# Optimization experiments

Hardware: AMD Instinct MI355X
Metric: run time of the kernel (lower is better)

The kernel has to match this reference:

```python
import jax, jax.numpy as jnp
import numpy as np

CHUNK = 32
FLOOR = 0.01
EPS_MIX = 1e-5
EPS_NORM = 1e-5


def l2norm(x):
    return x / jnp.sqrt(jnp.sum(x * x, -1, keepdims=True) + 1e-12)


def dw_causal_conv(x, w):
    # x: (B, L, C), w: (C, K) depthwise causal conv, tap K-1 is 'current'
    K = w.shape[-1]
    L = x.shape[1]
    xp = jnp.pad(x, ((0, 0), (K - 1, 0), (0, 0)))
    y = jnp.zeros_like(x)
    for t in range(K):
        y = y + xp[:, t:t + L, :] * w[:, t]
    return y


def delta_rule_chunkwise(q, k, v, beta):
    # q,k: (B,H,L,dk), v: (B,H,L,dv), beta: (B,H,L); L % CHUNK == 0
    b, h, L, dk = q.shape
    dv = v.shape[-1]
    c = CHUNK
    n = L // c
    q = l2norm(q)
    k = l2norm(k)
    v = v * beta[..., None]
    kb = k * beta[..., None]
    rs = lambda x: x.reshape(b, h, n, c, -1)
    qc, kc, vc, kbc = rs(q), rs(k), rs(v), rs(kb)
    # in-chunk inverse of (I + tril(K_beta K^T)) via forward substitution
    T = -jnp.einsum('bhnid,bhnjd->bhnij', kbc, kc)
    tri_strict = jnp.tril(jnp.ones((c, c), bool), -1)
    T = jnp.where(tri_strict, T, 0.0)
    for i in range(1, c):
        T = T.at[..., i, :i].add(
            jnp.einsum('bhnj,bhnji->bhni', T[..., i, :], T[..., :, :i]))
    T = T + jnp.eye(c, dtype=T.dtype)
    u = jnp.einsum('bhnij,bhnjd->bhnid', T, vc)
    w = jnp.einsum('bhnij,bhnjd->bhnid', T, kbc)
    mask_incl = jnp.tril(jnp.ones((c, c), bool), 0)

    def step(S, inp):
        qi, ki, ui, wi = inp  # each (b,h,c,d)
        attn = jnp.einsum('bhid,bhjd->bhij', qi, ki)
        attn = jnp.where(mask_incl, attn, 0.0)
        u_i = ui - jnp.einsum('bhik,bhkd->bhid', wi, S)
        o_i = jnp.einsum('bhik,bhkd->bhid', qi, S) + jnp.einsum('bhij,bhjd->bhid', attn, u_i)
        S = S + jnp.einsum('bhci,bhcd->bhid', ki, u_i)
        return S, o_i

    S0 = jnp.zeros((b, h, dk, dv), q.dtype)
    xs = tuple(jnp.moveaxis(a, 2, 0) for a in (qc, kc, u, w))
    S, o = jax.lax.scan(step, S0, xs)
    o = jnp.moveaxis(o, 0, 2).reshape(b, h, L, dv)
    return o, S


def setup_inputs() -> dict:
    key = jax.random.key(0)
    B, L, D, H = 4, 4096, 1024, 4
    dh = D // H  # 256
    ks = jax.random.split(key, 20)
    s = 1.0 / np.sqrt(D)
    inp = {
        'hidden_states': jax.random.normal(ks[0], (B, L, D), jnp.float32),
        'Wq': jax.random.normal(ks[1], (D, D), jnp.float32) * s,
        'Wk': jax.random.normal(ks[2], (D, D), jnp.float32) * s,
        'Wv': jax.random.normal(ks[3], (D, D), jnp.float32) * s,
        'Wb': jax.random.normal(ks[4], (D, H), jnp.float32) * s,
        'conv_q_w': jax.random.normal(ks[5], (D, 4), jnp.float32) * 0.5,
        'conv_k_w': jax.random.normal(ks[6], (D, 4), jnp.float32) * 0.5,
        'conv_v_w': jax.random.normal(ks[7], (D, 4), jnp.float32) * 0.5,
        'local_w': (jax.random.normal(ks[8], (H * dh, 7), jnp.float32) / np.sqrt(7.0)).at[:, -1].add(1.0),
        'mid_w': (jax.random.normal(ks[9], (H * dh, 25), jnp.float32) / np.sqrt(25.0)).at[:, -1].add(1.0),
        'r_w1': jax.random.normal(ks[10], (D + 14 * H, 2 * (D + 14 * H)), jnp.float32) / np.sqrt(D + 14 * H),
        'r_b1': jnp.zeros((2 * (D + 14 * H),), jnp.float32),
        'r_w2': jax.random.normal(ks[11], (2 * (D + 14 * H), H * 4), jnp.float32) / np.sqrt(2.0 * (D + 14 * H)),
        'r_b2': jnp.zeros((H, 4), jnp.float32).at[:, 2:].set(0.7).reshape(-1),
        'mix_w': jnp.ones((H, dh), jnp.float32),
        'onorm_w': jnp.ones((dh,), jnp.float32),
        'Wo': jax.random.normal(ks[12], (D, D), jnp.float32) * s,
    }
    return inp


def reference(hidden_states, Wq, Wk, Wv, Wb, conv_q_w, conv_k_w, conv_v_w,
              local_w, mid_w, r_w1, r_b1, r_w2, r_b2, mix_w, onorm_w, Wo):
    B, L, D = hidden_states.shape
    H = mix_w.shape[0]
    dh = mix_w.shape[1]
    # projections + short causal depthwise convs with SiLU (qk_activation='silu')
    q = jax.nn.silu(dw_causal_conv(hidden_states @ Wq, conv_q_w))
    k = jax.nn.silu(dw_causal_conv(hidden_states @ Wk, conv_k_w))
    v = jax.nn.silu(dw_causal_conv(hidden_states @ Wv, conv_v_w))
    q4 = q.reshape(B, L, H, dh)
    k4 = k.reshape(B, L, H, dh)
    v4 = v.reshape(B, L, H, dh)
    beta = jax.nn.sigmoid(hidden_states @ Wb)  # (B,L,H)
    delta_out, _ = delta_rule_chunkwise(
        jnp.transpose(q4, (0, 2, 1, 3)), jnp.transpose(k4, (0, 2, 1, 3)),
        jnp.transpose(v4, (0, 2, 1, 3)), jnp.transpose(beta, (0, 2, 1)))
    delta_out = jnp.transpose(delta_out, (0, 2, 1, 3))  # (B,L,H,dh)
    v_direct = v4
    vflat = v4.reshape(B, L, H * dh)
    local_out = dw_causal_conv(vflat, local_w).reshape(B, L, H, dh)
    mid_out = dw_causal_conv(vflat, mid_w).reshape(B, L, H, dh)
    outs = [local_out, mid_out, delta_out, v_direct]
    # router stats: per-head mean/var of each path + pairwise mean dots
    feats = []
    for o_ in outs:
        feats.append(o_.mean(-1))
        feats.append(jnp.var(o_, -1, ddof=1))
    for i in range(4):
        for j in range(i + 1, 4):
            feats.append((outs[i] * outs[j]).mean(-1))
    router_feat = jnp.concatenate([hidden_states] + feats, axis=-1)  # (B,L,D+14H)
    h1 = jax.nn.silu(router_feat @ r_w1 + r_b1)
    logits = (h1 @ r_w2 + r_b2).reshape(B, L, H, 4)
    p = jax.nn.softmax(logits, -1)
    p = p * (1.0 - 4.0 * FLOOR) + FLOOR  # probability floor
    mixed = sum(p[..., i:i + 1] * outs[i] for i in range(4))  # (B,L,H,dh)
    # MixNorm: per-token per-head RMSNorm with (H,dh) affine
    rms = jnp.sqrt(jnp.mean(mixed * mixed, -1, keepdims=True) + EPS_MIX)
    mixed = mixed / rms * mix_w
    # output RMSNorm (per head_v_dim)
    rms2 = jnp.sqrt(jnp.mean(mixed * mixed, -1, keepdims=True) + EPS_NORM)
    o_n = mixed / rms2 * onorm_w
    return o_n.reshape(B, L, H * dh) @ Wo
```

## Files before the change

kernel.cpp:

```cpp
#include <hip/hip_runtime.h>
#include <cstdint>
#include <cstddef>

typedef unsigned short u16;
typedef __bf16 bf16x8 __attribute__((ext_vector_type(8)));
typedef float    f32x4 __attribute__((ext_vector_type(4)));
typedef unsigned short u16x8 __attribute__((ext_vector_type(8)));
typedef unsigned short u16x4 __attribute__((ext_vector_type(4)));

#define MFMA16(a,b,c) __builtin_amdgcn_mfma_f32_16x16x32_bf16(a,b,c,0,0,0)

__device__ __forceinline__ float bf2f(u16 u){ return __uint_as_float(((unsigned)u)<<16); }
__device__ __forceinline__ u16 f2bf(float f){
  unsigned x = __float_as_uint(f);
  unsigned r = x + 0x7fffu + ((x>>16)&1u);
  return (u16)(r>>16);
}
__device__ __forceinline__ float wred(float v){
  #pragma unroll
  for (int o=32;o;o>>=1) v += __shfl_xor(v,o,64);
  return v;
}
__device__ __forceinline__ float siluf(float x){ return x/(1.f+__expf(-x)); }

__global__ __launch_bounds__(256) void k_zero(float* __restrict__ p, int n){
  int i = blockIdx.x*256 + threadIdx.x;
  if (i < n) p[i] = 0.f;
}

__global__ __launch_bounds__(256) void k_cvt(const float* __restrict__ src,
                                             u16* __restrict__ dst, int n){
  int i = (blockIdx.x*256 + threadIdx.x)*4;
  if (i < n){
    float4 f = *(const float4*)(src + i);
    u16x4 o; o[0]=f2bf(f.x); o[1]=f2bf(f.y); o[2]=f2bf(f.z); o[3]=f2bf(f.w);
    *(u16x4*)(dst + i) = o;
  }
}

__global__ __launch_bounds__(256) void k_tr(const float* __restrict__ src, u16* __restrict__ dst,
                                            int R, int C, int Rp, int Cp){
  __shared__ float t[32][33];
  int n0 = blockIdx.x*32, k0 = blockIdx.y*32;
  int tx = threadIdx.x & 31, ty = threadIdx.x >> 5;
  #pragma unroll
  for (int j=0;j<4;j++){
    int k = k0 + ty + j*8, nn = n0 + tx;
    t[ty + j*8][tx] = (k < R && nn < C) ? src[k*C + nn] : 0.f;
  }
  __syncthreads();
  #pragma unroll
  for (int j=0;j<4;j++){
    int nn = n0 + ty + j*8, k = k0 + tx;
    dst[nn*Rp + k] = f2bf(t[tx][ty + j*8]);
  }
}

__global__ __launch_bounds__(256) void k_pad_w2t(const float* __restrict__ src, u16* __restrict__ dst){
  int k = blockIdx.x*256 + threadIdx.x;
  int j = blockIdx.y;
  if (k < 2176) dst[j*2176 + k] = (k < 2160) ? f2bf(src[k*16 + j]) : (u16)0;
}
__global__ __launch_bounds__(256) void k_pad_b1(const float* __restrict__ src, float* __restrict__ dst){
  int i = blockIdx.x*256 + threadIdx.x;
  if (i < 2176) dst[i] = (i<2160) ? src[i] : 0.f;
}

__global__ __launch_bounds__(256) void k_trk(const u16* __restrict__ kn, u16* __restrict__ kTb){
  __shared__ u16 vs[32][264];
  const int g = blockIdx.x;
  const int bh = g >> 7, nc = g & 127;
  const int b = bh >> 2, h = bh & 3;
  const int tid = threadIdx.x;
  const int rr = tid >> 3, cb = (tid & 7) * 32;
  const u16* src = kn + (size_t)(b*4096 + nc*32 + rr)*1024 + h*256 + cb;
  #pragma unroll
  for (int v=0; v<4; ++v){
    u16x8 x = *(const u16x8*)(src + v*8);
    *(u16x8*)&vs[rr][cb + v*8] = x;
  }
  __syncthreads();
  u16* dst = kTb + ((size_t)g*256 + tid)*32;
  #pragma unroll
  for (int v=0; v<4; ++v){
    u16x8 o;
    #pragma unroll
    for (int e=0; e<8; e++) o[e] = vs[v*8 + e][tid];
    *(u16x8*)(dst + v*8) = o;
  }
}

__global__ __launch_bounds__(256,2) void k_gemm(
    const u16* __restrict__ A, const u16* __restrict__ Bt, void* __restrict__ Cvp,
    int M, int N, int K, int out_f32)
{
  __shared__ u16 As[2][128*64];
  __shared__ u16 Bs[2][128*64];
  const int tid = threadIdx.x;
  const int lane = tid & 63, wv = tid >> 6;
  const int wm = (wv>>1)*64, wn = (wv&1)*64;
  const int r15 = lane & 15, q4 = lane >> 4;
  const int bm0 = blockIdx.y*128, bn0 = blockIdx.x*128;
  const int srow = tid>>3, sch = tid&7;
  const int nk = K >> 6;

  const f32x4 fz = {0.f,0.f,0.f,0.f};
  f32x4 acc[4][4];
  #pragma unroll
  for (int i=0;i<4;i++){
    #pragma unroll
    for (int j=0;j<4;j++) acc[i][j] = fz;
  }

  {
    u16x8 ca[4], cb[4];
    #pragma unroll
    for (int i=0;i<4;i++){
      int r = i*32 + srow;
      ca[i] = *(const u16x8*)(A  + (size_t)(bm0+r)*K + sch*8);
      cb[i] = *(const u16x8*)(Bt + (size_t)(bn0+r)*K + sch*8);
    }
    #pragma unroll
    for (int i=0;i<4;i++){
      int r = i*32 + srow;
      int byt = r*128 + ((sch ^ (r&7))*16);
      *(u16x8*)((char*)(&As[0][0]) + byt) = ca[i];
      *(u16x8*)((char*)(&Bs[0][0]) + byt) = cb[i];
    }
  }
  int cur = 0;
  for (int t=0; t<nk; ++t){
    u16x8 na[4], nb[4];
    if (t+1 < nk){
      const int kt = (t+1)<<6;
      #pragma unroll
      for (int i=0;i<4;i++){
        int r = i*32 + srow;
        na[i] = *(const u16x8*)(A  + (size_t)(bm0+r)*K + kt + sch*8);
        nb[i] = *(const u16x8*)(Bt + (size_t)(bn0+r)*K + kt + sch*8);
      }
    }
    __syncthreads();
    const u16* as_ = &As[cur][0];
    const u16* bs_ = &Bs[cur][0];
    #pragma unroll
    for (int kk=0; kk<2; ++kk){
      bf16x8 av[4], bv[4];
      #pragma unroll
      for (int mi=0;mi<4;mi++){
        int row = wm + mi*16 + r15;
        int ch  = kk*4 + q4;
        av[mi] = *(const bf16x8*)((const char*)as_ + row*128 + ((ch ^ (row&7))*16));
      }
      #pragma unroll
      for (int ni=0;ni<4;ni++){
        int row = wn + ni*16 + r15;
        int ch  = kk*4 + q4;
        bv[ni] = *(const bf16x8*)((const char*)bs_ + row*128 + ((ch ^ (row&7))*16));
      }
      #pragma unroll
      for (int mi=0;mi<4;mi++){
        #pragma unroll
        for (int ni=0;ni<4;ni++)
          acc[mi][ni] = MFMA16(av[mi], bv[ni], acc[mi][ni]);
      }
    }
    if (t+1 < nk){
      #pragma unroll
      for (int i=0;i<4;i++){
        int r = i*32 + srow;
        int byt = r*128 + ((sch ^ (r&7))*16);
        *(u16x8*)((char*)(&As[cur^1][0]) + byt) = na[i];
        *(u16x8*)((char*)(&Bs[cur^1][0]) + byt) = nb[i];
      }
    }
    cur ^= 1;
  }
  float* Cf = (float*)Cvp;
  u16*  Cb2 = (u16*)Cvp;
  #pragma unroll
  for (int mi=0;mi<4;mi++){
    #pragma unroll
    for (int ni=0;ni<4;ni++){
      int gr = bm0 + wm + mi*16 + q4*4;
      int gc = bn0 + wn + ni*16 + r15;
      #pragma unroll
      for (int rg=0; rg<4; ++rg){
        float v = acc[mi][ni][rg];
        size_t off = (size_t)(gr+rg)*N + gc;
        if (out_f32) Cf[off] = v; else Cb2[off] = f2bf(v);
      }
    }
  }
}

union SMu {
  struct { u16 As[2][128*64]; u16 Bs[2][128*64]; } g;
  u16 h1s[128][136];
};
__global__ __launch_bounds__(256,2) void k_gemm_router(
    const u16* __restrict__ A, const u16* __restrict__ Bt,
    const float* __restrict__ bias, const u16* __restrict__ w2t,
    float* __restrict__ logits)
{
  __shared__ SMu sm;
  const int tid = threadIdx.x;
  const int lane = tid & 63, wv = tid >> 6;
  const int wm = (wv>>1)*64, wn = (wv&1)*64;
  const int r15 = lane & 15, q4 = lane >> 4;
  const int bm0 = blockIdx.y*128, bn0 = blockIdx.x*128;
  const int srow = tid>>3, sch = tid&7;
  const int K = 1088, nk = 17;

  const f32x4 fz = {0.f,0.f,0.f,0.f};
  f32x4 acc[4][4];
  #pragma unroll
  for (int i=0;i<4;i++){
    #pragma unroll
    for (int j=0;j<4;j++) acc[i][j] = fz;
  }
  {
    u16x8 ca[4], cb[4];
    #pragma unroll
    for (int i=0;i<4;i++){
      int r = i*32 + srow;
      ca[i] = *(const u16x8*)(A  + (size_t)(bm0+r)*K + sch*8);
      cb[i] = *(const u16x8*)(Bt + (size_t)(bn0+r)*K + sch*8);
    }
    #pragma unroll
    for (int i=0;i<4;i++){
      int r = i*32 + srow;
      int byt = r*128 + ((sch ^ (r&7))*16);
      *(u16x8*)((char*)(&sm.g.As[0][0]) + byt) = ca[i];
      *(u16x8*)((char*)(&sm.g.Bs[0][0]) + byt) = cb[i];
    }
  }
  int cur = 0;
  for (int t=0; t<nk; ++t){
    u16x8 na[4], nb[4];
    if (t+1 < nk){
      const int kt = (t+1)<<6;
      #pragma unroll
      for (int i=0;i<4;i++){
        int r = i*32 + srow;
        na[i] = *(const u16x8*)(A  + (size_t)(bm0+r)*K + kt + sch*8);
        nb[i] = *(const u16x8*)(Bt + (size_t)(bn0+r)*K + kt + sch*8);
      }
    }
    __syncthreads();
    const u16* as_ = &sm.g.As[cur][0];
    const u16* bs_ = &sm.g.Bs[cur][0];
    #pragma unroll
    for (int kk=0; kk<2; ++kk){
      bf16x8 av[4], bv[4];
      #pragma unroll
      for (int mi=0;mi<4;mi++){
        int row = wm + mi*16 + r15;
        int ch  = kk*4 + q4;
        av[mi] = *(const bf16x8*)((const char*)as_ + row*128 + ((ch ^ (row&7))*16));
      }
      #pragma unroll
      for (int ni=0;ni<4;ni++){
        int row = wn + ni*16 + r15;
        int ch  = kk*4 + q4;
        bv[ni] = *(const bf16x8*)((const char*)bs_ + row*128 + ((ch ^ (row&7))*16));
      }
      #pragma unroll
      for (int mi=0;mi<4;mi++){
        #pragma unroll
        for (int ni=0;ni<4;ni++)
          acc[mi][ni] = MFMA16(av[mi], bv[ni], acc[mi][ni]);
      }
    }
    if (t+1 < nk){
      #pragma unroll
      for (int i=0;i<4;i++){
        int r = i*32 + srow;
        int byt = r*128 + ((sch ^ (r&7))*16);
        *(u16x8*)((char*)(&sm.g.As[cur^1][0]) + byt) = na[i];
        *(u16x8*)((char*)(&sm.g.Bs[cur^1][0]) + byt) = nb[i];
      }
    }
    cur ^= 1;
  }
  __syncthreads();
  #pragma unroll
  for (int mi=0;mi<4;mi++){
    #pragma unroll
    for (int ni=0;ni<4;ni++){
      int lr = wm + mi*16 + q4*4;
      int lc = wn + ni*16 + r15;
      float bv_ = bias[bn0 + lc];
      #pragma unroll
      for (int rg=0; rg<4; ++rg)
        sm.h1s[lr+rg][lc] = f2bf(siluf(acc[mi][ni][rg] + bv_));
    }
  }
  __syncthreads();
  f32x4 lacc[2] = {fz, fz};
  #pragma unroll
  for (int rt=0; rt<2; ++rt){
    #pragma unroll
    for (int ks=0; ks<4; ++ks){
      bf16x8 a = *(const bf16x8*)((const char*)&sm.h1s[wv*32 + rt*16 + r15][0] + ks*64 + q4*16);
      bf16x8 b = *(const bf16x8*)(w2t + r15*2176 + bn0 + ks*32 + q4*8);
      lacc[rt] = MFMA16(a, b, lacc[rt]);
    }
  }
  #pragma unroll
  for (int rt=0; rt<2; ++rt){
    #pragma unroll
    for (int rg=0; rg<4; ++rg){
      int m = bm0 + wv*32 + rt*16 + q4*4 + rg;
      atomicAdd(&logits[m*16 + r15], lacc[rt][rg]);
    }
  }
}

__global__ __launch_bounds__(256) void k_softm(float* __restrict__ p, const float* __restrict__ b2){
  int m = blockIdx.x*256 + threadIdx.x;
  float l[16];
  #pragma unroll
  for (int j=0;j<16;j++) l[j] = p[m*16+j] + b2[j];
  #pragma unroll
  for (int hh=0;hh<4;hh++){
    float l0=l[hh*4+0], l1=l[hh*4+1], l2=l[hh*4+2], l3=l[hh*4+3];
    float mx = fmaxf(fmaxf(l0,l1),fmaxf(l2,l3));
    float e0=__expf(l0-mx), e1=__expf(l1-mx), e2=__expf(l2-mx), e3=__expf(l3-mx);
    float iv = 1.f/(e0+e1+e2+e3);
    p[m*16+hh*4+0]=e0*iv*0.96f+0.01f;
    p[m*16+hh*4+1]=e1*iv*0.96f+0.01f;
    p[m*16+hh*4+2]=e2*iv*0.96f+0.01f;
    p[m*16+hh*4+3]=e3*iv*0.96f+0.01f;
  }
}

__global__ __launch_bounds__(256) void k_beta(const u16* __restrict__ Xb,
                                              const float* __restrict__ Wb,
                                              float* __restrict__ beta){
  int m = blockIdx.x*4 + (threadIdx.x>>6);
  int lane = threadIdx.x & 63;
  float a0=0.f,a1=0.f,a2=0.f,a3=0.f;
  #pragma unroll 4
  for (int i=0;i<16;i++){
    int k = lane + i*64;
    float x = bf2f(Xb[m*1024 + k]);
    float4 wr = *(const float4*)(Wb + k*4);
    a0 += x*wr.x; a1 += x*wr.y; a2 += x*wr.z; a3 += x*wr.w;
  }
  a0 = wred(a0); a1 = wred(a1); a2 = wred(a2); a3 = wred(a3);
  if (lane == 0){
    beta[m*4+0] = 1.f/(1.f+__expf(-a0));
    beta[m*4+1] = 1.f/(1.f+__expf(-a1));
    beta[m*4+2] = 1.f/(1.f+__expf(-a2));
    beta[m*4+3] = 1.f/(1.f+__expf(-a3));
  }
}

__global__ __launch_bounds__(256) void k_conv(const u16* __restrict__ raw,
                                              const float* __restrict__ cw,
                                              u16* __restrict__ outp, int do_norm){
  const int m = blockIdx.x;
  const int tid = threadIdx.x, lane = tid&63, hh = tid>>6;
  const int l = m & 4095;
  const int cbase = hh*256 + lane*4;
  float x[4][4];
  #pragma unroll
  for (int j=0;j<4;j++){
    if (l >= j){
      u16x4 xv = *(const u16x4*)(raw + (m-j)*1024 + cbase);
      #pragma unroll
      for (int e=0;e<4;e++) x[j][e] = bf2f(xv[e]);
    } else {
      #pragma unroll
      for (int e=0;e<4;e++) x[j][e] = 0.f;
    }
  }
  float y[4]; float ss = 0.f;
  #pragma unroll
  for (int e=0;e<4;e++){
    int c = cbase + e;
    float yy = x[0][e]*cw[c*4+3] + x[1][e]*cw[c*4+2] + x[2][e]*cw[c*4+1] + x[3][e]*cw[c*4+0];
    yy = siluf(yy);
    y[e] = yy; ss += yy*yy;
  }
  if (do_norm){
    ss = wred(ss);
    float sc = rsqrtf(ss + 1e-12f);
    #pragma unroll
    for (int e=0;e<4;e++) y[e] *= sc;
  }
  u16x4 o;
  #pragma unroll
  for (int e=0;e<4;e++) o[e] = f2bf(y[e]);
  *(u16x4*)(outp + m*1024 + cbase) = o;
}

__global__ __launch_bounds__(256) void k_localmid(const u16* __restrict__ v,
                                                  const float* __restrict__ lw,
                                                  const float* __restrict__ mw,
                                                  u16* __restrict__ lo, u16* __restrict__ mo){
  __shared__ u16 vs[56][256];
  const int lt0 = blockIdx.x*32;
  const int b = blockIdx.y;
  const int c0 = blockIdx.z*256;
  const int tid = threadIdx.x;
  #pragma unroll
  for (int i=0;i<7;i++){
    int flat = tid + i*256;
    int row = flat >> 5;
    int cc = (flat & 31)*8;
    int tok = lt0 - 24 + row;
    u16x8 val = {0,0,0,0,0,0,0,0};
    if (tok >= 0) val = *(const u16x8*)(v + (b*4096 + tok)*1024 + c0 + cc);
    *(u16x8*)&vs[row][cc] = val;
  }
  __syncthreads();
  const int c = tid;
  float lwr[7], mwr[25];
  #pragma unroll
  for (int i=0;i<7;i++) lwr[i] = lw[(c0+c)*7 + i];
  #pragma unroll
  for (int i=0;i<25;i++) mwr[i] = mw[(c0+c)*25 + i];
  for (int lt=0; lt<32; ++lt){
    float a7=0.f, a25=0.f;
    #pragma unroll
    for (int t=0;t<25;t++) a25 += bf2f(vs[lt+t][c]) * mwr[t];
    #pragma unroll
    for (int t=0;t<7;t++)  a7  += bf2f(vs[18+lt+t][c]) * lwr[t];
    int m = b*4096 + lt0 + lt;
    lo[m*1024 + c0 + c] = f2bf(a7);
    mo[m*1024 + c0 + c] = f2bf(a25);
  }
}

__global__ __launch_bounds__(256,2) void k_chunk(
    const u16* __restrict__ qn, const u16* __restrict__ kn, const u16* __restrict__ v,
    const float* __restrict__ beta, u16* __restrict__ u_, u16* __restrict__ w_,
    u16* __restrict__ attnb)
{
  const int chk = blockIdx.x;
  const int nc = chk & 127;
  const int bh = chk >> 7;
  const int b = bh >> 2, h = bh & 3;
  const int tok0 = b*4096 + nc*32;
  const int tid = threadIdx.x, lane = tid&63, wv = tid>>6;
  const int r15 = lane&15, q4 = lane>>4;

  __shared__ u16 kbT[256][40];
  __shared__ u16 vbT[256][40];
  __shared__ float Tm[4][32][33];
  __shared__ u16 Xs[32][40];

  {
    int rr = tid >> 3;
    int cb = (tid & 7)*32;
    float bt = beta[(tok0 + rr)*4 + h];
    const u16* ksrc = kn + (tok0+rr)*1024 + h*256 + cb;
    const u16* vsrc = v  + (tok0+rr)*1024 + h*256 + cb;
    #pragma unroll
    for (int vvv=0; vvv<4; ++vvv){
      u16x8 kx = *(const u16x8*)(ksrc + vvv*8);
      u16x8 vx = *(const u16x8*)(vsrc + vvv*8);
      #pragma unroll
      for (int e=0;e<8;e++){
        kbT[cb + vvv*8 + e][rr] = f2bf(bf2f(kx[e]) * bt);
        vbT[cb + vvv*8 + e][rr] = f2bf(bf2f(vx[e]) * bt);
      }
    }
  }
  {
    const int i0 = (wv>>1)*16, j0 = (wv&1)*16;
    float bi = beta[(tok0 + i0 + r15)*4 + h];
    f32x4 tacc = {0.f,0.f,0.f,0.f};
    #pragma unroll
    for (int ks=0; ks<8; ++ks){
      u16x8 ar = *(const u16x8*)(kn + (tok0 + i0 + r15)*1024 + h*256 + ks*32 + q4*8);
      union { u16x8 u; bf16x8 bf; } au;
      #pragma unroll
      for (int e=0;e<8;e++) au.u[e] = f2bf(bf2f(ar[e]) * bi);
      bf16x8 bv = *(const bf16x8*)(kn + (tok0 + j0 + r15)*1024 + h*256 + ks*32 + q4*8);
      tacc = MFMA16(au.bf, bv, tacc);
    }
    #pragma unroll
    for (int rg=0; rg<4; ++rg){
      int i = i0 + q4*4 + rg, j = j0 + r15;
      float val = (i > j) ? -tacc[rg] : 0.f;
      Tm[0][i][j] = val;
      Tm[2][i][j] = val + ((i==j)?1.f:0.f);
    }
  }
  __syncthreads();
  int cbuf = 0, cx = 2;
  const int ii = tid >> 3, jj = (tid&7)*4;
  for (int s=0; s<4; ++s){
    int nb = cbuf^1, nx = cx^1;
    {
      float o0=0.f,o1=0.f,o2=0.f,o3=0.f;
      for (int k=0;k<32;k++){
        float a = Tm[cbuf][ii][k];
        o0 += a*Tm[cbuf][k][jj+0]; o1 += a*Tm[cbuf][k][jj+1];
        o2 += a*Tm[cbuf][k][jj+2]; o3 += a*Tm[cbuf][k][jj+3];
      }
      Tm[nb][ii][jj+0]=o0; Tm[nb][ii][jj+1]=o1; Tm[nb][ii][jj+2]=o2; Tm[nb][ii][jj+3]=o3;
    }
    __syncthreads();
    {
      float o0=Tm[cx][ii][jj+0], o1=Tm[cx][ii][jj+1], o2=Tm[cx][ii][jj+2], o3=Tm[cx][ii][jj+3];
      for (int k=0;k<32;k++){
        float a = Tm[nb][ii][k];
        o0 += a*Tm[cx][k][jj+0]; o1 += a*Tm[cx][k][jj+1];
        o2 += a*Tm[cx][k][jj+2]; o3 += a*Tm[cx][k][jj+3];
      }
      Tm[nx][ii][jj+0]=o0; Tm[nx][ii][jj+1]=o1; Tm[nx][ii][jj+2]=o2; Tm[nx][ii][jj+3]=o3;
    }
    __syncthreads();
    cbuf = nb; cx = nx;
  }
  {
    #pragma unroll
    for (int e=0;e<4;e++) Xs[ii][jj+e] = f2bf(Tm[cx][ii][jj+e]);
  }
  __syncthreads();
  {
    #pragma unroll
    for (int nt=0; nt<4; ++nt){
      int n0 = wv*64 + nt*16;
      #pragma unroll
      for (int mt=0; mt<2; ++mt){
        bf16x8 a = *(const bf16x8*)((const char*)&Xs[mt*16 + r15][0] + q4*16);
        bf16x8 bu = *(const bf16x8*)((const char*)&vbT[n0 + r15][0] + q4*16);
        bf16x8 bw = *(const bf16x8*)((const char*)&kbT[n0 + r15][0] + q4*16);
        f32x4 ua = {0.f,0.f,0.f,0.f};
        f32x4 wa = {0.f,0.f,0.f,0.f};
        ua = MFMA16(a, bu, ua);
        wa = MFMA16(a, bw, wa);
        #pragma unroll
        for (int rg=0;rg<4;rg++){
          int row = mt*16 + q4*4 + rg;
          int col = n0 + r15;
          u_[(chk*32 + row)*256 + col] = f2bf(ua[rg]);
          w_[(chk*32 + row)*256 + col] = f2bf(wa[rg]);
        }
      }
    }
  }
  {
    const int i0 = (wv>>1)*16, j0 = (wv&1)*16;
    f32x4 aacc = {0.f,0.f,0.f,0.f};
    #pragma unroll
    for (int ks=0;ks<8;++ks){
      bf16x8 a = *(const bf16x8*)(qn + (tok0 + i0 + r15)*1024 + h*256 + ks*32 + q4*8);
      bf16x8 bv = *(const bf16x8*)(kn + (tok0 + j0 + r15)*1024 + h*256 + ks*32 + q4*8);
      aacc = MFMA16(a, bv, aacc);
    }
    #pragma unroll
    for (int rg=0;rg<4;rg++){
      int i = i0 + q4*4 + rg, j = j0 + r15;
      attnb[chk*1024 + i*32 + j] = f2bf((i>=j)? aacc[rg] : 0.f);
    }
  }
}

struct ScanCtx { u16x8 kf[4]; u16x8 wf[8]; u16x8 at; u16 uv[4]; };

#define SBAR() do{ asm volatile("s_waitcnt lgkmcnt(0)" ::: "memory"); \
                   __builtin_amdgcn_s_barrier(); \
                   asm volatile("" ::: "memory"); }while(0)

#define SPREF(C, CHK) { \
  const u16* kp = kTb + ((size_t)(CHK)*256 + wv*64 + r15)*32 + q4*8; \
  _Pragma("unroll") for (int mt=0;mt<4;++mt) C.kf[mt] = *(const u16x8*)(kp + mt*512); \
  const u16* wp = w_ + ((size_t)(CHK)*32 + tm*16 + r15)*256 + q4*8; \
  _Pragma("unroll") for (int ks=0;ks<8;++ks) C.wf[ks] = *(const u16x8*)(wp + ks*32); \
  C.at = *(const u16x8*)(attnb + (size_t)(CHK)*1024 + (tm*16 + r15)*32 + q4*8); \
  const u16* up = u_ + ((size_t)(CHK)*32 + tm*16 + q4*4)*256 + dv0 + tn*16 + r15; \
  _Pragma("unroll") for (int rg=0;rg<4;++rg) C.uv[rg] = up[rg*256]; \
}

#define SBODY(C, N, NC, CB, NB) { \
  const int chkn_ = chkbase + (((NC)+1 < 128) ? (NC)+1 : 127); \
  SPREF(N, chkn_); \
  u16x8 qf[8]; \
  { const u16* qp = qn + (size_t)(tokbase + (NC)*32 + tm*16 + r15)*1024 + h*256 + q4*8; \
    _Pragma("unroll") for (int ks=0;ks<8;++ks) qf[ks] = *(const u16x8*)(qp + ks*32); } \
  bf16x8 sf[8]; \
  _Pragma("unroll") for (int ks=0;ks<8;++ks) \
    sf[ks] = *(const bf16x8*)((const char*)&Sb[CB][tn*16 + r15][0] + ks*64 + q4*16); \
  f32x4 ua = fz, ub = fz; \
  _Pragma("unroll") for (int ks=0;ks<8;ks+=2){ \
    ua = MFMA16(*(const bf16x8*)&C.wf[ks],   sf[ks],   ua); \
    ub = MFMA16(*(const bf16x8*)&C.wf[ks+1], sf[ks+1], ub); } \
  { u16x4 pk; \
    _Pragma("unroll") for (int rg=0;rg<4;++rg) pk[rg] = f2bf(bf2f(C.uv[rg]) - ua[rg] - ub[rg]); \
    *(u16x4*)&uT[tn*16 + r15][tm*16 + q4*4] = pk; } \
  SBAR(); \
  bf16x8 bu0 = *(const bf16x8*)((const char*)&uT[r15][0] + q4*16); \
  bf16x8 bu1 = *(const bf16x8*)((const char*)&uT[16 + r15][0] + q4*16); \
  f32x4 oa = fz, ob = fz; \
  _Pragma("unroll") for (int ks=0;ks<8;ks+=2){ \
    oa = MFMA16(*(const bf16x8*)&qf[ks],   sf[ks],   oa); \
    ob = MFMA16(*(const bf16x8*)&qf[ks+1], sf[ks+1], ob); } \
  oa = MFMA16(*(const bf16x8*)&C.at, (tn ? bu1 : bu0), oa); \
  _Pragma("unroll") for (int rg=0;rg<4;++rg) \
    od[(size_t)(tokbase + (NC)*32 + tm*16 + q4*4 + rg)*1024 + h*256 + dv0 + tn*16 + r15] = f2bf(oa[rg] + ob[rg]); \
  _Pragma("unroll") for (int mt=0;mt<4;++mt){ \
    Sacc[mt][0] = MFMA16(*(const bf16x8*)&C.kf[mt], bu0, Sacc[mt][0]); \
    Sacc[mt][1] = MFMA16(*(const bf16x8*)&C.kf[mt], bu1, Sacc[mt][1]); } \
  _Pragma("unroll") for (int mt=0;mt<4;++mt){ \
    _Pragma("unroll") for (int ntl=0;ntl<2;++ntl){ \
      u16x4 pk; \
      _Pragma("unroll") for (int rg=0;rg<4;++rg) pk[rg] = f2bf(Sacc[mt][ntl][rg]); \
      *(u16x4*)&Sb[NB][ntl*16 + r15][wv*64 + mt*16 + q4*4] = pk; } } \
  SBAR(); \
}

__global__ __launch_bounds__(256,1) void k_scan(
    const u16* __restrict__ qn, const u16* __restrict__ kTb,
    const u16* __restrict__ u_, const u16* __restrict__ w_,
    const u16* __restrict__ attnb, u16* __restrict__ od)
{
  const int bid = blockIdx.x;
  const int bh  = (bid & 7) | (((bid >> 3) & 1) << 3);
  const int dv0 = (bid >> 4) * 32;
  const int b = bh >> 2, h = bh & 3;
  const int tid = threadIdx.x, lane = tid & 63, wv = tid >> 6;
  const int tm = wv >> 1, tn = wv & 1;
  const int r15 = lane & 15, q4 = lane >> 4;
  const int chkbase = bh * 128;
  const int tokbase = b * 4096;

  __shared__ u16 Sb[2][32][264];
  __shared__ u16 uT[32][40];

  for (int i = tid; i < 2*32*264; i += 256) (&Sb[0][0][0])[i] = 0;
  const f32x4 fz = {0.f,0.f,0.f,0.f};
  f32x4 Sacc[4][2];
  #pragma unroll
  for (int a_=0;a_<4;a_++){
    #pragma unroll
    for (int b_=0;b_<2;b_++) Sacc[a_][b_] = fz;
  }
  ScanCtx cA, cB;
  SPREF(cA, chkbase);
  __syncthreads();

  for (int nc = 0; nc < 128; nc += 2){
    SBODY(cA, cB, nc,   0, 1)
    SBODY(cB, cA, nc+1, 1, 0)
  }
}

__global__ __launch_bounds__(256) void k_feats(
    const float* __restrict__ Xf, const u16* __restrict__ lo, const u16* __restrict__ mo,
    const u16* __restrict__ de, const u16* __restrict__ vv, u16* __restrict__ feat)
{
  const int m = blockIdx.x;
  const int tid = threadIdx.x, lane = tid & 63, hh = tid >> 6;
  {
    float4 xv = *(const float4*)(Xf + m*1024 + tid*4);
    u16x4 o; o[0]=f2bf(xv.x); o[1]=f2bf(xv.y); o[2]=f2bf(xv.z); o[3]=f2bf(xv.w);
    *(u16x4*)(feat + m*1088 + tid*4) = o;
  }
  if (tid < 8) feat[m*1088 + 1080 + tid] = 0;
  const int base = m*1024 + hh*256 + lane*4;
  u16x4 a0 = *(const u16x4*)(lo + base);
  u16x4 a1 = *(const u16x4*)(mo + base);
  u16x4 a2 = *(const u16x4*)(de + base);
  u16x4 a3 = *(const u16x4*)(vv + base);
  float s[14];
  #pragma unroll
  for (int i=0;i<14;i++) s[i]=0.f;
  #pragma unroll
  for (int e=0;e<4;e++){
    float L = bf2f(a0[e]), Mm = bf2f(a1[e]), D = bf2f(a2[e]), V = bf2f(a3[e]);
    s[0]+=L; s[1]+=L*L; s[2]+=Mm; s[3]+=Mm*Mm; s[4]+=D; s[5]+=D*D; s[6]+=V; s[7]+=V*V;
    s[8]+=L*Mm; s[9]+=L*D; s[10]+=L*V; s[11]+=Mm*D; s[12]+=Mm*V; s[13]+=D*V;
  }
  #pragma unroll
  for (int i=0;i<14;i++) s[i] = wred(s[i]);
  if (lane == 0){
    const float inv = 1.f/256.f, invv = 1.f/255.f;
    u16* fb = feat + m*1088 + 1024;
    float mn[4] = {s[0]*inv, s[2]*inv, s[4]*inv, s[6]*inv};
    float vr[4] = {(s[1]-256.f*mn[0]*mn[0])*invv, (s[3]-256.f*mn[1]*mn[1])*invv,
                   (s[5]-256.f*mn[2]*mn[2])*invv, (s[7]-256.f*mn[3]*mn[3])*invv};
    #pragma unroll
    for (int i=0;i<4;i++){ fb[(2*i)*4 + hh] = f2bf(mn[i]); fb[(2*i+1)*4 + hh] = f2bf(vr[i]); }
    #pragma unroll
    for (int i=0;i<6;i++) fb[(8+i)*4 + hh] = f2bf(s[8+i]*inv);
  }
}

__global__ __launch_bounds__(256) void k_mix(
    const u16* __restrict__ lo, const u16* __restrict__ mo, const u16* __restrict__ de,
    const u16* __restrict__ vv, const float* __restrict__ p,
    const float* __restrict__ mixw, const float* __restrict__ onw, u16* __restrict__ on)
{
  const int m = blockIdx.x;
  const int tid = threadIdx.x, lane = tid&63, hh = tid>>6;
  const int dbase = lane*4;
  const int base = m*1024 + hh*256 + dbase;
  float4 pv = *(const float4*)(p + m*16 + hh*4);
  u16x4 a0 = *(const u16x4*)(lo + base);
  u16x4 a1 = *(const u16x4*)(mo + base);
  u16x4 a2 = *(const u16x4*)(de + base);
  u16x4 a3 = *(const u16x4*)(vv + base);
  float g[4]; float ss = 0.f;
  #pragma unroll
  for (int e=0;e<4;e++){
    float x = pv.x*bf2f(a0[e]) + pv.y*bf2f(a1[e]) + pv.z*bf2f(a2[e]) + pv.w*bf2f(a3[e]);
    g[e]=x; ss += x*x;
  }
  ss = wred(ss);
  float r1 = rsqrtf(ss*(1.f/256.f) + 1e-5f);
  float ss2 = 0.f;
  #pragma unroll
  for (int e=0;e<4;e++){ g[e] = g[e]*r1*mixw[hh*256 + dbase + e]; ss2 += g[e]*g[e]; }
  ss2 = wred(ss2);
  float r2 = rsqrtf(ss2*(1.f/256.f) + 1e-5f);
  u16x4 o;
  #pragma unroll
  for (int e=0;e<4;e++) o[e] = f2bf(g[e]*r2*onw[dbase + e]);
  *(u16x4*)(on + base) = o;
}

extern "C" void kernel_launch(void* const* d_in, const int* in_sizes, int n_in,
                              void* d_out, int out_size, void* d_ws, size_t ws_size,
                              hipStream_t stream)
{
  const float* X   = (const float*)d_in[0];
  const float* Wq  = (const float*)d_in[1];
  const float* Wk  = (const float*)d_in[2];
  const float* Wv  = (const float*)d_in[3];
  const float* Wb  = (const float*)d_in[4];
  const float* cqw = (const float*)d_in[5];
  const float* ckw = (const float*)d_in[6];
  const float* cvw = (const float*)d_in[7];
  const float* lw  = (const float*)d_in[8];
  const float* mw  = (const float*)d_in[9];
  const float* rw1 = (const float*)d_in[10];
  const float* rb1 = (const float*)d_in[11];
  const float* rw2 = (const float*)d_in[12];
  const float* rb2 = (const float*)d_in[13];
  const float* mixw= (const float*)d_in[14];
  const float* onw = (const float*)d_in[15];
  const float* Wo  = (const float*)d_in[16];

  char* ws = (char*)d_ws;
  const size_t SLOT = 33554432;
  char* s0 = ws;
  char* s1 = ws + 1*SLOT;
  char* s2 = ws + 2*SLOT;
  char* s3 = ws + 3*SLOT;
  char* s4 = ws + 4*SLOT;
  char* s5 = ws + 5*SLOT;
  char* s6 = ws + 6*SLOT;
  char* ext = ws + 7*SLOT;
  u16*   attb  = (u16*)(ext);
  float* pb    = (float*)(ext + 4194304);
  float* betab = (float*)(ext + 4194304 + 1048576);
  char*  wsp   = ext + 4194304 + 1048576 + 262144;
  u16* Wqt = (u16*)(wsp);
  u16* Wkt = (u16*)(wsp + 2097152);
  u16* Wvt = (u16*)(wsp + 2*2097152);
  u16* Wot = (u16*)(wsp + 3*2097152);
  u16* w1t = (u16*)(wsp + 4*2097152);
  u16* w2t = (u16*)(wsp + 4*2097152 + 4734976);
  float* b1p = (float*)(wsp + 4*2097152 + 4734976 + 69632);

  u16* Xb    = (u16*)s0;
  u16* rawb  = (u16*)s1;
  u16* qnb   = (u16*)s2;
  u16* knb   = (u16*)s3;
  u16* vpb   = (u16*)s4;
  u16* ub    = (u16*)s0;
  u16* wbuf  = (u16*)s1;
  u16* odb   = (u16*)s5;
  u16* kTbp  = (u16*)s6;
  u16* lob   = (u16*)s2;
  u16* mob   = (u16*)s3;
  u16* featb = (u16*)s0;
  u16* onb   = (u16*)s0;

  k_zero<<<1024,256,0,stream>>>(pb, 262144);
  k_cvt<<<16384,256,0,stream>>>(X, Xb, 16777216);
  k_tr<<<dim3(32,32),256,0,stream>>>(Wq, Wqt, 1024,1024,1024,1024);
  k_tr<<<dim3(32,32),256,0,stream>>>(Wk, Wkt, 1024,1024,1024,1024);
  k_tr<<<dim3(32,32),256,0,stream>>>(Wv, Wvt, 1024,1024,1024,1024);
  k_tr<<<dim3(32,32),256,0,stream>>>(Wo, Wot, 1024,1024,1024,1024);
  k_tr<<<dim3(68,34),256,0,stream>>>(rw1, w1t, 1080,2160,1088,2176);
  k_pad_w2t<<<dim3(9,16),256,0,stream>>>(rw2, w2t);
  k_pad_b1<<<9,256,0,stream>>>(rb1, b1p);
  k_gemm<<<dim3(8,128),256,0,stream>>>(Xb, Wqt, rawb, 16384,1024,1024, 0);
  k_conv<<<16384,256,0,stream>>>(rawb, cqw, qnb, 1);
  k_gemm<<<dim3(8,128),256,0,stream>>>(Xb, Wkt, rawb, 16384,1024,1024, 0);
  k_conv<<<16384,256,0,stream>>>(rawb, ckw, knb, 1);
  k_gemm<<<dim3(8,128),256,0,stream>>>(Xb, Wvt, rawb, 16384,1024,1024, 0);
  k_conv<<<16384,256,0,stream>>>(rawb, cvw, vpb, 0);
  k_beta<<<4096,256,0,stream>>>(Xb, Wb, betab);
  k_chunk<<<2048,256,0,stream>>>(qnb, knb, vpb, betab, ub, wbuf, attb);
  k_trk<<<2048,256,0,stream>>>(knb, kTbp);
  k_scan<<<128,256,0,stream>>>(qnb, kTbp, ub, wbuf, attb, odb);
  k_localmid<<<dim3(128,4,4),256,0,stream>>>(vpb, lw, mw, lob, mob);
  k_feats<<<16384,256,0,stream>>>(X, lob, mob, odb, vpb, featb);
  k_gemm_router<<<dim3(17,128),256,0,stream>>>(featb, w1t, b1p, w2t, pb);
  k_softm<<<64,256,0,stream>>>(pb, rb2);
  k_mix<<<16384,256,0,stream>>>(lob, mob, odb, vpb, pb, mixw, onw, onb);
  k_gemm<<<dim3(8,128),256,0,stream>>>(onb, Wot, d_out, 16384,1024,1024, 1);
}
```

Before: 1.149 ms.

## Merge 32-token chunks into 128-token superchunks for delta-rule scan

Adds compose kernels that merge adjacent chunk-local u/w (WY) representations hierarchically, 32 to 64 to 128, so the sequential scan runs 32 steps of 128 tokens instead of 128 steps of 32. A new kernel computes the causal 128x128 q·k attention as lower-triangular 16x16 tiles, and the scan is split into 256 blocks of 16 value columns for more parallelism. The serial dependency chain of the recurrent state shrinks, in exchange for extra compose passes, more bf16 rounding in the composed u/w, and a reworked workspace layout that reuses the ext region for the transposed Wq/Wk/Wv weights.

```diff
diff --git a/kernel.cpp b/kernel.cpp
--- a/kernel.cpp
+++ b/kernel.cpp
@@ -111,7 +111,6 @@
     #pragma unroll
     for (int j=0;j<4;j++) acc[i][j] = fz;
   }
-
   {
     u16x8 ca[4], cb[4];
     #pragma unroll
@@ -436,8 +435,7 @@
 
 __global__ __launch_bounds__(256,2) void k_chunk(
     const u16* __restrict__ qn, const u16* __restrict__ kn, const u16* __restrict__ v,
-    const float* __restrict__ beta, u16* __restrict__ u_, u16* __restrict__ w_,
-    u16* __restrict__ attnb)
+    const float* __restrict__ beta, u16* __restrict__ u_, u16* __restrict__ w_)
 {
   const int chk = blockIdx.x;
   const int nc = chk & 127;
@@ -545,109 +543,195 @@
       }
     }
   }
+}
+
+__global__ __launch_bounds__(256,2) void k_attn128(const u16* __restrict__ qn,
+                                                   const u16* __restrict__ kn,
+                                                   u16* __restrict__ att){
+  const int g = blockIdx.x;
+  const int bh = g >> 5, sc = g & 31;
+  const int b = bh >> 2, h = bh & 3;
+  const int tid = threadIdx.x, lane = tid&63, wv = tid>>6;
+  const int r15 = lane&15, q4 = lane>>4;
+  const int tok0 = b*4096 + sc*128;
+  const f32x4 fz = {0.f,0.f,0.f,0.f};
+  u16* base = att + (size_t)g*36*256;
+  #pragma unroll
+  for (int ti=0; ti<8; ++ti){
+    #pragma unroll
+    for (int tj=0; tj<=ti; ++tj){
+      if (((ti+tj)&3) != wv) continue;
+      f32x4 acc = fz;
+      const u16* qp = qn + (size_t)(tok0 + ti*16 + r15)*1024 + h*256 + q4*8;
+      const u16* kp = kn + (size_t)(tok0 + tj*16 + r15)*1024 + h*256 + q4*8;
+      #pragma unroll
+      for (int ks=0; ks<8; ++ks)
+        acc = MFMA16(*(const bf16x8*)(qp + ks*32), *(const bf16x8*)(kp + ks*32), acc);
+      u16* op = base + (size_t)(((ti*(ti+1))>>1) + tj)*256;
+      #pragma unroll
+      for (int rg=0; rg<4; ++rg){
+        float vv = acc[rg];
+        if (ti==tj && r15 > q4*4+rg) vv = 0.f;
+        op[(q4*4+rg)*16 + r15] = f2bf(vv);
+      }
+    }
+  }
+}
+
+template<int HS>
+__global__ __launch_bounds__(256,1) void k_compose(const u16* __restrict__ kn,
+                                                   u16* __restrict__ u_,
+                                                   u16* __restrict__ w_){
+  const int g = blockIdx.x;
+  const int ppb = 2048/HS;
+  const int bh = g / ppb, pr = g % ppb;
+  const int b = bh>>2, h = bh&3;
+  const int ta = pr*2*HS, tb2 = ta + HS;
+  const int tid = threadIdx.x, lane = tid&63, wv = tid>>6;
+  const int r15 = lane&15, q4 = lane>>4;
+  __shared__ u16 uaT[256][HS+8];
+  __shared__ u16 waT[256][HS+8];
+  __shared__ u16 Ms[HS][HS+8];
+  const f32x4 fz = {0.f,0.f,0.f,0.f};
   {
-    const int i0 = (wv>>1)*16, j0 = (wv&1)*16;
-    f32x4 aacc = {0.f,0.f,0.f,0.f};
-    #pragma unroll
-    for (int ks=0;ks<8;++ks){
-      bf16x8 a = *(const bf16x8*)(qn + (tok0 + i0 + r15)*1024 + h*256 + ks*32 + q4*8);
-      bf16x8 bv = *(const bf16x8*)(kn + (tok0 + j0 + r15)*1024 + h*256 + ks*32 + q4*8);
-      aacc = MFMA16(a, bv, aacc);
-    }
-    #pragma unroll
-    for (int rg=0;rg<4;rg++){
-      int i = i0 + q4*4 + rg, j = j0 + r15;
-      attnb[chk*1024 + i*32 + j] = f2bf((i>=j)? aacc[rg] : 0.f);
-    }
-  }
-}
-
-struct ScanCtx { u16x8 kf[4]; u16x8 wf[8]; u16x8 at; u16 uv[4]; };
+    const int tpr = 256/HS;
+    const int jr = tid / tpr;
+    const int dg = (tid % tpr) * HS;
+    const u16* us = u_ + (size_t)(bh*4096 + ta + jr)*256 + dg;
+    const u16* wsc = w_ + (size_t)(bh*4096 + ta + jr)*256 + dg;
+    #pragma unroll
+    for (int e0=0; e0<HS; e0+=8){
+      u16x8 xu = *(const u16x8*)(us + e0);
+      u16x8 xw = *(const u16x8*)(wsc + e0);
+      #pragma unroll
+      for (int e=0;e<8;e++){ uaT[dg+e0+e][jr] = xu[e]; waT[dg+e0+e][jr] = xw[e]; }
+    }
+  }
+  constexpr int NT = HS/16;
+  for (int t = wv; t < NT*NT; t += 4){
+    int ti = t / NT, tj = t % NT;
+    f32x4 acc = fz;
+    const u16* ap = w_ + (size_t)(bh*4096 + tb2 + ti*16 + r15)*256 + q4*8;
+    const u16* bp = kn + (size_t)(b*4096 + ta + tj*16 + r15)*1024 + h*256 + q4*8;
+    #pragma unroll
+    for (int ks=0; ks<8; ++ks)
+      acc = MFMA16(*(const bf16x8*)(ap + ks*32), *(const bf16x8*)(bp + ks*32), acc);
+    #pragma unroll
+    for (int rg=0; rg<4; ++rg)
+      Ms[ti*16 + q4*4 + rg][tj*16 + r15] = f2bf(acc[rg]);
+  }
+  __syncthreads();
+  for (int t = wv; t < NT*16; t += 4){
+    int ti = t >> 4, nj = t & 15;
+    f32x4 aU = fz, aW = fz;
+    #pragma unroll
+    for (int js=0; js<HS/32; ++js){
+      bf16x8 a  = *(const bf16x8*)((const char*)&Ms[ti*16 + r15][0] + js*64 + q4*16);
+      bf16x8 bu = *(const bf16x8*)((const char*)&uaT[nj*16 + r15][0] + js*64 + q4*16);
+      bf16x8 bw = *(const bf16x8*)((const char*)&waT[nj*16 + r15][0] + js*64 + q4*16);
+      aU = MFMA16(a, bu, aU);
+      aW = MFMA16(a, bw, aW);
+    }
+    #pragma unroll
+    for (int rg=0; rg<4; ++rg){
+      size_t off = (size_t)(bh*4096 + tb2 + ti*16 + q4*4 + rg)*256 + nj*16 + r15;
+      u_[off] = f2bf(bf2f(u_[off]) - aU[rg]);
+      w_[off] = f2bf(bf2f(w_[off]) - aW[rg]);
+    }
+  }
+}
+
+struct Pref { u16x8 wf[2][8]; u16x4 uv[2]; };
 
 #define SBAR() do{ asm volatile("s_waitcnt lgkmcnt(0)" ::: "memory"); \
                    __builtin_amdgcn_s_barrier(); \
                    asm volatile("" ::: "memory"); }while(0)
 
-#define SPREF(C, CHK) { \
-  const u16* kp = kTb + ((size_t)(CHK)*256 + wv*64 + r15)*32 + q4*8; \
-  _Pragma("unroll") for (int mt=0;mt<4;++mt) C.kf[mt] = *(const u16x8*)(kp + mt*512); \
-  const u16* wp = w_ + ((size_t)(CHK)*32 + tm*16 + r15)*256 + q4*8; \
-  _Pragma("unroll") for (int ks=0;ks<8;++ks) C.wf[ks] = *(const u16x8*)(wp + ks*32); \
-  C.at = *(const u16x8*)(attnb + (size_t)(CHK)*1024 + (tm*16 + r15)*32 + q4*8); \
-  const u16* up = u_ + ((size_t)(CHK)*32 + tm*16 + q4*4)*256 + dv0 + tn*16 + r15; \
-  _Pragma("unroll") for (int rg=0;rg<4;++rg) C.uv[rg] = up[rg*256]; \
-}
-
-#define SBODY(C, N, NC, CB, NB) { \
-  const int chkn_ = chkbase + (((NC)+1 < 128) ? (NC)+1 : 127); \
-  SPREF(N, chkn_); \
-  u16x8 qf[8]; \
-  { const u16* qp = qn + (size_t)(tokbase + (NC)*32 + tm*16 + r15)*1024 + h*256 + q4*8; \
-    _Pragma("unroll") for (int ks=0;ks<8;++ks) qf[ks] = *(const u16x8*)(qp + ks*32); } \
+#define SPREF128(C, SC) { \
+  _Pragma("unroll") for (int rt=0; rt<2; ++rt){ \
+    const u16* wp = w_ + (size_t)(ubase + (SC)*128 + (wv*2+rt)*16 + r15)*256 + q4*8; \
+    _Pragma("unroll") for (int ks=0; ks<8; ++ks) C.wf[rt][ks] = *(const u16x8*)(wp + ks*32); \
+    const u16* up = u_ + (size_t)(ubase + (SC)*128 + (wv*2+rt)*16 + q4*4)*256 + dv0 + r15; \
+    u16x4 t_; \
+    _Pragma("unroll") for (int rg=0; rg<4; ++rg) t_[rg] = up[rg*256]; \
+    C.uv[rt] = t_; } }
+
+#define SBODY128(C, N, SC, CB, NB) { \
+  { const int scn = ((SC)+1 < 32) ? (SC)+1 : 31; SPREF128(N, scn); } \
+  u16x8 kf[4][4]; \
+  _Pragma("unroll") for (int mt=0; mt<4; ++mt) \
+    _Pragma("unroll") for (int sl=0; sl<4; ++sl) \
+      kf[mt][sl] = *(const u16x8*)(kTb + ((size_t)(chkbase + (SC)*4 + sl)*256 + wv*64 + mt*16 + r15)*32 + q4*8); \
+  u16x8 at[2][4]; u16x8 qf[2][8]; \
+  _Pragma("unroll") for (int rt=0; rt<2; ++rt){ \
+    const int R = wv*2+rt; \
+    const u16* ab = att + (size_t)((bh*32 + (SC))*36 + ((R*(R+1))>>1))*256 + r15*16 + (q4&1)*8; \
+    _Pragma("unroll") for (int js=0; js<4; ++js){ \
+      if (js <= (R>>1)){ \
+        int tj = 2*js + (q4>>1); \
+        u16x8 z = {0,0,0,0,0,0,0,0}; \
+        at[rt][js] = (tj <= R) ? *(const u16x8*)(ab + (size_t)tj*256) : z; } } \
+    const u16* qp = qn + (size_t)(qbase + (SC)*128 + R*16 + r15)*1024 + h*256 + q4*8; \
+    _Pragma("unroll") for (int ks=0; ks<8; ++ks) qf[rt][ks] = *(const u16x8*)(qp + ks*32); } \
   bf16x8 sf[8]; \
-  _Pragma("unroll") for (int ks=0;ks<8;++ks) \
-    sf[ks] = *(const bf16x8*)((const char*)&Sb[CB][tn*16 + r15][0] + ks*64 + q4*16); \
-  f32x4 ua = fz, ub = fz; \
-  _Pragma("unroll") for (int ks=0;ks<8;ks+=2){ \
-    ua = MFMA16(*(const bf16x8*)&C.wf[ks],   sf[ks],   ua); \
-    ub = MFMA16(*(const bf16x8*)&C.wf[ks+1], sf[ks+1], ub); } \
-  { u16x4 pk; \
-    _Pragma("unroll") for (int rg=0;rg<4;++rg) pk[rg] = f2bf(bf2f(C.uv[rg]) - ua[rg] - ub[rg]); \
-    *(u16x4*)&uT[tn*16 + r15][tm*16 + q4*4] = pk; } \
+  _Pragma("unroll") for (int ks=0; ks<8; ++ks) \
+    sf[ks] = *(const bf16x8*)((const char*)&Sb[CB][r15][0] + ks*64 + q4*16); \
+  _Pragma("unroll") for (int rt=0; rt<2; ++rt){ \
+    f32x4 ua = fz; \
+    _Pragma("unroll") for (int ks=0; ks<8; ++ks) ua = MFMA16(*(const bf16x8*)&C.wf[rt][ks], sf[ks], ua); \
+    u16x4 pk; \
+    _Pragma("unroll") for (int rg=0; rg<4; ++rg) pk[rg] = f2bf(bf2f(C.uv[rt][rg]) - ua[rg]); \
+    *(u16x4*)&uT[r15][(wv*2+rt)*16 + q4*4] = pk; } \
   SBAR(); \
-  bf16x8 bu0 = *(const bf16x8*)((const char*)&uT[r15][0] + q4*16); \
-  bf16x8 bu1 = *(const bf16x8*)((const char*)&uT[16 + r15][0] + q4*16); \
-  f32x4 oa = fz, ob = fz; \
-  _Pragma("unroll") for (int ks=0;ks<8;ks+=2){ \
-    oa = MFMA16(*(const bf16x8*)&qf[ks],   sf[ks],   oa); \
-    ob = MFMA16(*(const bf16x8*)&qf[ks+1], sf[ks+1], ob); } \
-  oa = MFMA16(*(const bf16x8*)&C.at, (tn ? bu1 : bu0), oa); \
-  _Pragma("unroll") for (int rg=0;rg<4;++rg) \
-    od[(size_t)(tokbase + (NC)*32 + tm*16 + q4*4 + rg)*1024 + h*256 + dv0 + tn*16 + r15] = f2bf(oa[rg] + ob[rg]); \
-  _Pragma("unroll") for (int mt=0;mt<4;++mt){ \
-    Sacc[mt][0] = MFMA16(*(const bf16x8*)&C.kf[mt], bu0, Sacc[mt][0]); \
-    Sacc[mt][1] = MFMA16(*(const bf16x8*)&C.kf[mt], bu1, Sacc[mt][1]); } \
-  _Pragma("unroll") for (int mt=0;mt<4;++mt){ \
-    _Pragma("unroll") for (int ntl=0;ntl<2;++ntl){ \
-      u16x4 pk; \
-      _Pragma("unroll") for (int rg=0;rg<4;++rg) pk[rg] = f2bf(Sacc[mt][ntl][rg]); \
-      *(u16x4*)&Sb[NB][ntl*16 + r15][wv*64 + mt*16 + q4*4] = pk; } } \
-  SBAR(); \
-}
-
-__global__ __launch_bounds__(256,1) void k_scan(
+  bf16x8 bu[4]; \
+  _Pragma("unroll") for (int sl=0; sl<4; ++sl) \
+    bu[sl] = *(const bf16x8*)((const char*)&uT[r15][0] + sl*64 + q4*16); \
+  _Pragma("unroll") for (int rt=0; rt<2; ++rt){ \
+    const int R = wv*2+rt; \
+    f32x4 oa = fz; \
+    _Pragma("unroll") for (int ks=0; ks<8; ++ks) oa = MFMA16(*(const bf16x8*)&qf[rt][ks], sf[ks], oa); \
+    _Pragma("unroll") for (int js=0; js<4; ++js) \
+      if (js <= (R>>1)) oa = MFMA16(*(const bf16x8*)&at[rt][js], bu[js], oa); \
+    _Pragma("unroll") for (int rg=0; rg<4; ++rg) \
+      od[(size_t)(qbase + (SC)*128 + R*16 + q4*4 + rg)*1024 + h*256 + dv0 + r15] = f2bf(oa[rg]); } \
+  _Pragma("unroll") for (int mt=0; mt<4; ++mt){ \
+    _Pragma("unroll") for (int sl=0; sl<4; ++sl) \
+      Sacc[mt] = MFMA16(*(const bf16x8*)&kf[mt][sl], bu[sl], Sacc[mt]); \
+    u16x4 pk; \
+    _Pragma("unroll") for (int rg=0; rg<4; ++rg) pk[rg] = f2bf(Sacc[mt][rg]); \
+    *(u16x4*)&Sb[NB][r15][wv*64 + mt*16 + q4*4] = pk; } \
+  SBAR(); }
+
+__global__ __launch_bounds__(256,1) void k_scan128(
     const u16* __restrict__ qn, const u16* __restrict__ kTb,
     const u16* __restrict__ u_, const u16* __restrict__ w_,
-    const u16* __restrict__ attnb, u16* __restrict__ od)
+    const u16* __restrict__ att, u16* __restrict__ od)
 {
   const int bid = blockIdx.x;
   const int bh  = (bid & 7) | (((bid >> 3) & 1) << 3);
-  const int dv0 = (bid >> 4) * 32;
+  const int dv0 = (bid >> 4) * 16;
   const int b = bh >> 2, h = bh & 3;
   const int tid = threadIdx.x, lane = tid & 63, wv = tid >> 6;
-  const int tm = wv >> 1, tn = wv & 1;
   const int r15 = lane & 15, q4 = lane >> 4;
   const int chkbase = bh * 128;
-  const int tokbase = b * 4096;
-
-  __shared__ u16 Sb[2][32][264];
-  __shared__ u16 uT[32][40];
-
-  for (int i = tid; i < 2*32*264; i += 256) (&Sb[0][0][0])[i] = 0;
+  const int ubase = bh * 4096;
+  const int qbase = b * 4096;
+
+  __shared__ u16 Sb[2][16][264];
+  __shared__ u16 uT[16][136];
+
+  for (int i = tid; i < 2*16*264; i += 256) (&Sb[0][0][0])[i] = 0;
   const f32x4 fz = {0.f,0.f,0.f,0.f};
-  f32x4 Sacc[4][2];
-  #pragma unroll
-  for (int a_=0;a_<4;a_++){
-    #pragma unroll
-    for (int b_=0;b_<2;b_++) Sacc[a_][b_] = fz;
-  }
-  ScanCtx cA, cB;
-  SPREF(cA, chkbase);
+  f32x4 Sacc[4];
+  #pragma unroll
+  for (int mt=0; mt<4; ++mt) Sacc[mt] = fz;
+  Pref cA, cB;
+  SPREF128(cA, 0);
   __syncthreads();
 
-  for (int nc = 0; nc < 128; nc += 2){
-    SBODY(cA, cB, nc,   0, 1)
-    SBODY(cB, cA, nc+1, 1, 0)
+  for (int sc = 0; sc < 32; sc += 2){
+    SBODY128(cA, cB, sc,   0, 1)
+    SBODY128(cB, cA, sc+1, 1, 0)
   }
 }
 
@@ -757,17 +841,17 @@
   char* s5 = ws + 5*SLOT;
   char* s6 = ws + 6*SLOT;
   char* ext = ws + 7*SLOT;
-  u16*   attb  = (u16*)(ext);
-  float* pb    = (float*)(ext + 4194304);
-  float* betab = (float*)(ext + 4194304 + 1048576);
-  char*  wsp   = ext + 4194304 + 1048576 + 262144;
-  u16* Wqt = (u16*)(wsp);
-  u16* Wkt = (u16*)(wsp + 2097152);
-  u16* Wvt = (u16*)(wsp + 2*2097152);
-  u16* Wot = (u16*)(wsp + 3*2097152);
-  u16* w1t = (u16*)(wsp + 4*2097152);
-  u16* w2t = (u16*)(wsp + 4*2097152 + 4734976);
-  float* b1p = (float*)(wsp + 4*2097152 + 4734976 + 69632);
+  u16*   att128 = (u16*)(ext);
+  float* pb    = (float*)(ext + 9437184);
+  float* betab = (float*)(ext + 9437184 + 1048576);
+  char*  wsp   = ext + 9437184 + 1048576 + 262144;
+  u16* Wot = (u16*)(wsp);
+  u16* w1t = (u16*)(wsp + 2097152);
+  u16* w2t = (u16*)(wsp + 2097152 + 4734976);
+  float* b1p = (float*)(wsp + 2097152 + 4734976 + 69632);
+  u16* Wqt = (u16*)(ext);
+  u16* Wkt = (u16*)(ext + 2097152);
+  u16* Wvt = (u16*)(ext + 4194304);
 
   u16* Xb    = (u16*)s0;
   u16* rawb  = (u16*)s1;
@@ -799,9 +883,12 @@
   k_gemm<<<dim3(8,128),256,0,stream>>>(Xb, Wvt, rawb, 16384,1024,1024, 0);
   k_conv<<<16384,256,0,stream>>>(rawb, cvw, vpb, 0);
   k_beta<<<4096,256,0,stream>>>(Xb, Wb, betab);
-  k_chunk<<<2048,256,0,stream>>>(qnb, knb, vpb, betab, ub, wbuf, attb);
+  k_chunk<<<2048,256,0,stream>>>(qnb, knb, vpb, betab, ub, wbuf);
+  k_attn128<<<512,256,0,stream>>>(qnb, knb, att128);
   k_trk<<<2048,256,0,stream>>>(knb, kTbp);
-  k_scan<<<128,256,0,stream>>>(qnb, kTbp, ub, wbuf, attb, odb);
+  k_compose<32><<<1024,256,0,stream>>>(knb, ub, wbuf);
+  k_compose<64><<<512,256,0,stream>>>(knb, ub, wbuf);
+  k_scan128<<<256,256,0,stream>>>(qnb, kTbp, ub, wbuf, att128, odb);
   k_localmid<<<dim3(128,4,4),256,0,stream>>>(vpb, lw, mw, lob, mob);
   k_feats<<<16384,256,0,stream>>>(X, lob, mob, odb, vpb, featb);
   k_gemm_router<<<dim3(17,128),256,0,stream>>>(featb, w1t, b1p, w2t, pb);
```

Measured after the change: 1.084 ms. 5.7% less time.
